# Performance work log

Measured on AMD Instinct MI355X. Metric: run time of the kernel, lower is better.

The kernel has to match this reference:

```python
import jax, jax.numpy as jnp
import numpy as np


def setup_inputs() -> dict:
    key = jax.random.key(0)
    k1, k2, k3, k4, k5 = jax.random.split(key, 5)
    N, M, K = 200000, 50, 4
    T = 1000.0
    ti = jnp.sort(jax.random.uniform(k1, (N,), dtype=jnp.float32) * T)
    mi = jax.random.randint(k2, (N,), 0, M, dtype=jnp.int64)
    mu_at_events = jax.random.uniform(k3, (N,), dtype=jnp.float32) * 0.5 + 0.05
    alpha = jax.random.uniform(k4, (K, M, M), dtype=jnp.float32) * 0.1
    gamma = jax.random.uniform(k5, (K,), dtype=jnp.float32) * 2.0 + 0.5
    return {"ti": ti, "mi": mi, "mu_at_events": mu_at_events, "alpha": alpha, "gamma": gamma}


def _hawkes_logsum(ti, mi, mu_at_events, alpha, gamma):
    # ti: [N] sorted event times; mi: [N] event types in [0, M)
    # alpha: [K, M, M]; gamma: [K]; mu_at_events: [N]
    N = ti.shape[0]
    M = alpha.shape[1]
    # inter-event gaps; dt[0] = 0 so the first event has zero excitation state
    dt = jnp.concatenate([jnp.zeros((1,), ti.dtype), ti[1:] - ti[:-1]])  # [N]
    a = jnp.exp(-gamma[None, :] * dt[:, None])  # [N, K] decay factors
    # one-hot of the PREVIOUS event's type (row 0 is all-zero, matching e_mi)
    prev_onehot = jnp.zeros((N, M), ti.dtype).at[jnp.arange(1, N), mi[:-1]].set(1.0)
    b = a[:, None, :] * prev_onehot[:, :, None]  # [N, M, K]

    # linear recurrence S_i = a_i * S_{i-1} + b_i via associative scan
    # combine((a1,b1),(a2,b2)) = (a1*a2, a2*b1 + b2)
    def combine(x, y):
        a1, b1 = x
        a2, b2 = y
        return (a1 * a2, a2[:, None, :] * b1 + b2)

    _, S = jax.lax.associative_scan(combine, (a, b))  # S: [N, M, K]
    # S[i, m, k] = sum_{j < i, m_j = m} exp(-gamma_k (t_i - t_j))
    alpha_at = alpha[:, mi, :]  # [K, N, M] rows of alpha for each event's type
    lam = mu_at_events + jnp.einsum('knm,nmk,k->n', alpha_at, S, gamma)  # [N]
    return jnp.sum(jnp.log(lam))


def reference(ti, mi, mu_at_events, alpha, gamma):
    return _hawkes_logsum(ti, mi, mu_at_events, alpha, gamma)
```

## Files before the change

### kernel.cpp

```cpp
#include <hip/hip_runtime.h>

#define CHUNK 256
#define MM 50
#define KK 4
#define STATE (MM*KK)
#define ASTRIDE 51
#define SUP 32
#define NSMAX 26
#define NSUB 8
#define SUBSZ 32
#define GMAX 1024

__device__ int      g_ticket;
__device__ unsigned g_flag[GMAX];
__device__ unsigned g_sflag[64];
__device__ float    g_chunkB[GMAX * STATE];
__device__ float    g_superB[64 * STATE];

__device__ __forceinline__ unsigned short f2bf(float x) {
  unsigned u = __float_as_uint(x);
  u += 0x7fffu + ((u >> 16) & 1u);
  return (unsigned short)(u >> 16);
}
__device__ __forceinline__ float bflo(unsigned u) { return __uint_as_float(u << 16); }
__device__ __forceinline__ float bfhi(unsigned u) { return __uint_as_float(u & 0xffff0000u); }

__device__ __forceinline__ void st_agent(float* p, float v) {
  __hip_atomic_store(p, v, __ATOMIC_RELAXED, __HIP_MEMORY_SCOPE_AGENT);
}
__device__ __forceinline__ float ld_agent(const float* p) {
  return __hip_atomic_load(p, __ATOMIC_RELAXED, __HIP_MEMORY_SCOPE_AGENT);
}

__global__ __launch_bounds__(512) void hawkes_fused(
    const float* __restrict__ ti, const int* __restrict__ mi,
    const float* __restrict__ mu, const float* __restrict__ alpha,
    const float* __restrict__ gamma, float* __restrict__ out, int N, int G) {
  int tid = threadIdx.x;
  __shared__ int vid_s;
  __shared__ uint2 P[MM * ASTRIDE];
  __shared__ __align__(16) float4 Fj[CHUNK];
  __shared__ int   cj[CHUNK];
  __shared__ __align__(16) float Q[NSUB][STATE];
  __shared__ float red8[8];
  __shared__ float teL[SUP];
  __shared__ float tlast[NSMAX];
  __shared__ float S_lds[STATE];
  __shared__ __align__(16) float R_lds[MM * 20];

  if (tid == 0) vid_s = atomicAdd(&g_ticket, 1);

  int g = blockIdx.x;
  int l = g * CHUNK;
  int r = min(N, l + CHUNK);
  int cnt = r - l;
  int sup = g / SUP;
  int g0 = sup * SUP;
  int e = tid >> 1;
  int h = tid & 1;

  float gk0 = gamma[0], gk1 = gamma[1], gk2 = gamma[2], gk3 = gamma[3];

  for (int i = tid; i < NSUB * STATE; i += 512) ((float*)Q)[i] = 0.f;

  if (tid < SUP) {
    int c = g0 + tid;
    if (c < G) teL[tid] = ti[min(N, (c + 1) * CHUNK) - 1];
  } else if (tid >= 64 && tid < 64 + NSMAX) {
    int s = tid - 64;
    if (s < sup) tlast[s] = ti[min(N, (s + 1) * SUP * CHUNK) - 1];
  }

  float t_ref = ti[(g == 0) ? 0 : (l - 1)];
  bool valid = false;
  int myc = 0;
  float4 myF = make_float4(0.f, 0.f, 0.f, 0.f);
  if (tid < CHUNK) {
    int j = l - 1 + tid;
    valid = (j >= 0) && (j <= r - 2);
    if (valid) {
      myc = mi[j];
      float tj = ti[j] - t_ref;
      myF = make_float4(__expf(gk0 * tj), __expf(gk1 * tj),
                        __expf(gk2 * tj), __expf(gk3 * tj));
    }
    cj[tid] = myc;
    Fj[tid] = myF;
  }
  __syncthreads();

  if (valid) {
    float* q = &Q[tid >> 5][myc * KK];
    atomicAdd(q + 0, myF.x); atomicAdd(q + 1, myF.y);
    atomicAdd(q + 2, myF.z); atomicAdd(q + 3, myF.w);
  }
  __syncthreads();

  float gk = (tid & 2) ? ((tid & 1) ? gk3 : gk2) : ((tid & 1) ? gk1 : gk0);
  float Bv = 0.f, t_end = 0.f;
  if (tid < STATE) {
    t_end = teL[g - g0];
    float tot = 0.f;
    #pragma unroll
    for (int q = 0; q < NSUB; ++q) tot += Q[q][tid];
    Bv = __expf(-gk * (t_end - t_ref)) * tot;
    st_agent(&g_chunkB[g * STATE + tid], Bv);
    float run = 0.f;
    #pragma unroll
    for (int q = 0; q < NSUB; ++q) {
      float tq = Q[q][tid];
      Q[q][tid] = run;
      run += tq;
    }
  }
  if (g == 0 && tid == 0) st_agent(out, 0.f);

  for (int idx = tid; idx < MM * MM; idx += 512) {
    int c = idx / MM, cp = idx - c * MM;
    float a0 = gk0 * alpha[idx];
    float a1 = gk1 * alpha[2500 + idx];
    float a2 = gk2 * alpha[5000 + idx];
    float a3 = gk3 * alpha[7500 + idx];
    P[c * ASTRIDE + cp] =
        make_uint2((unsigned)f2bf(a0) | ((unsigned)f2bf(a1) << 16),
                   (unsigned)f2bf(a2) | ((unsigned)f2bf(a3) << 16));
  }
  __syncthreads();
  unsigned DONE = (unsigned)(vid_s / G) + 1u;
  if (tid == 0) {
    asm volatile("s_waitcnt vmcnt(0)" ::: "memory");
    __hip_atomic_store(&g_flag[g], DONE, __ATOMIC_RELAXED, __HIP_MEMORY_SCOPE_AGENT);
  }

  int nloc = g - g0;
  bool closer = (nloc == SUP - 1) || (g == G - 1);
  float S = 0.f;

  if (closer) {
    if (tid < nloc) {
      while (__hip_atomic_load(&g_flag[g0 + tid], __ATOMIC_RELAXED,
                               __HIP_MEMORY_SCOPE_AGENT) != DONE)
        __builtin_amdgcn_s_sleep(2);
    }
    __syncthreads();
    if (tid < STATE) {
      #pragma unroll 8
      for (int u = 0; u < nloc; ++u)
        S += __expf(-gk * (t_ref - teL[u])) * ld_agent(&g_chunkB[(g0 + u) * STATE + tid]);
      st_agent(&g_superB[sup * STATE + tid], __expf(-gk * (t_end - t_ref)) * S + Bv);
    }
    __syncthreads();
    if (tid == 0) {
      asm volatile("s_waitcnt vmcnt(0)" ::: "memory");
      __hip_atomic_store(&g_sflag[sup], DONE, __ATOMIC_RELAXED, __HIP_MEMORY_SCOPE_AGENT);
    }
  }

  int c_n = (e < cnt) ? mi[l + e] : 0;
  int rowb = c_n * ASTRIDE;
  float tn = 0.f, mun = 0.f;
  if (h == 0 && e < cnt) { tn = ti[l + e] - t_ref; mun = mu[l + e]; }
  float4 acc = make_float4(0.f, 0.f, 0.f, 0.f);
  if (e < cnt) {
    const float4* wb = (const float4*)&Q[e >> 5][0];
    if (e >= SUBSZ) {
      int mlo = h * 25, mhi = mlo + 25;
      #pragma unroll 5
      for (int m = mlo; m < mhi; ++m) {
        uint2 p = P[rowb + m];
        float4 w = wb[m];
        acc.x += bflo(p.x) * w.x; acc.y += bfhi(p.x) * w.y;
        acc.z += bflo(p.y) * w.z; acc.w += bfhi(p.y) * w.w;
      }
    }
    #pragma unroll 4
    for (int s = (e & ~(SUBSZ - 1)) + h; s <= e; s += 2) {
      uint2 p = P[rowb + cj[s]];
      float4 f = Fj[s];
      acc.x += bflo(p.x) * f.x; acc.y += bfhi(p.x) * f.y;
      acc.z += bflo(p.y) * f.z; acc.w += bfhi(p.y) * f.w;
    }
  }
  acc.x += __shfl_xor(acc.x, 1, 64);
  acc.y += __shfl_xor(acc.y, 1, 64);
  acc.z += __shfl_xor(acc.z, 1, 64);
  acc.w += __shfl_xor(acc.w, 1, 64);

  if (!closer) {
    if (tid < nloc) {
      while (__hip_atomic_load(&g_flag[g0 + tid], __ATOMIC_RELAXED,
                               __HIP_MEMORY_SCOPE_AGENT) != DONE)
        __builtin_amdgcn_s_sleep(2);
    }
    __syncthreads();
    if (tid < STATE) {
      #pragma unroll 8
      for (int u = 0; u < nloc; ++u)
        S += __expf(-gk * (t_ref - teL[u])) * ld_agent(&g_chunkB[(g0 + u) * STATE + tid]);
    }
  }
  if (tid < sup) {
    while (__hip_atomic_load(&g_sflag[tid], __ATOMIC_RELAXED,
                             __HIP_MEMORY_SCOPE_AGENT) != DONE)
      __builtin_amdgcn_s_sleep(2);
  }
  __syncthreads();
  if (tid < STATE) {
    #pragma unroll 8
    for (int s = 0; s < sup; ++s)
      S += __expf(-gk * (t_ref - tlast[s])) * ld_agent(&g_superB[s * STATE + tid]);
    S_lds[tid] = S;
  }
  __syncthreads();

  if (tid < STATE) {
    int c = tid >> 2, k = tid & 3;
    float rv = 0.f;
    #pragma unroll 5
    for (int m = 0; m < MM; ++m) {
      uint2 p = P[c * ASTRIDE + m];
      unsigned w = (k & 2) ? p.y : p.x;
      float pv = (k & 1) ? bfhi(w) : bflo(w);
      rv += pv * S_lds[m * KK + k];
    }
    R_lds[c * 20 + k] = rv;
  }
  __syncthreads();

  float local = 0.f;
  if (h == 0 && e < cnt) {
    float4 rv = *(const float4*)&R_lds[c_n * 20];
    float lam = mun
              + __expf(-gk0 * tn) * (acc.x + rv.x)
              + __expf(-gk1 * tn) * (acc.y + rv.y)
              + __expf(-gk2 * tn) * (acc.z + rv.z)
              + __expf(-gk3 * tn) * (acc.w + rv.w);
    local = __logf(lam);
  }
  #pragma unroll
  for (int off = 32; off > 0; off >>= 1)
    local += __shfl_down(local, off, 64);
  if ((tid & 63) == 0) red8[tid >> 6] = local;
  __syncthreads();
  if (tid == 0) {
    float acc8 = 0.f;
    #pragma unroll
    for (int w = 0; w < 8; ++w) acc8 += red8[w];
    atomicAdd(out, acc8);
  }
}

extern "C" void kernel_launch(void* const* d_in, const int* in_sizes, int n_in,
                              void* d_out, int out_size, void* d_ws, size_t ws_size,
                              hipStream_t stream) {
  const float* ti    = (const float*)d_in[0];
  const int*   mi    = (const int*)d_in[1];
  const float* mu    = (const float*)d_in[2];
  const float* alpha = (const float*)d_in[3];
  const float* gamma = (const float*)d_in[4];
  float* out = (float*)d_out;
  int N = in_sizes[0];
  int G = (N + CHUNK - 1) / CHUNK;
  if (G > GMAX) return;

  hawkes_fused<<<G, 512, 0, stream>>>(ti, mi, mu, alpha, gamma, out, N, G);
}
```

Baseline: 94.00 us.

## Process two chunks per block with one thread per event

Each 512-thread block now handles two adjacent 256-event chunks, with one thread per event instead of two threads splitting each event's sum. The block count is halved. This shortens the cross-block flag chain, and the second chunk's carry-in state is derived locally from the first. The flag publish is also moved ahead of the alpha table build, so dependent blocks can start sooner. In exchange, each thread does twice the serial inner-loop work, which lengthens per-thread latency.

```diff
diff --git a/kernel.cpp b/kernel.cpp
--- a/kernel.cpp
+++ b/kernel.cpp
@@ -7,7 +7,6 @@
 #define ASTRIDE 51
 #define SUP 32
 #define NSMAX 26
-#define NSUB 8
 #define SUBSZ 32
 #define GMAX 1024
 
@@ -31,62 +30,71 @@
 __device__ __forceinline__ float ld_agent(const float* p) {
   return __hip_atomic_load(p, __ATOMIC_RELAXED, __HIP_MEMORY_SCOPE_AGENT);
 }
+__device__ __forceinline__ void spin_flag(unsigned* p, unsigned want) {
+  while (__hip_atomic_load(p, __ATOMIC_RELAXED, __HIP_MEMORY_SCOPE_AGENT) != want)
+    __builtin_amdgcn_s_sleep(2);
+}
 
 __global__ __launch_bounds__(512) void hawkes_fused(
     const float* __restrict__ ti, const int* __restrict__ mi,
     const float* __restrict__ mu, const float* __restrict__ alpha,
-    const float* __restrict__ gamma, float* __restrict__ out, int N, int G) {
+    const float* __restrict__ gamma, float* __restrict__ out,
+    int N, int G, int NB) {
   int tid = threadIdx.x;
   __shared__ int vid_s;
   __shared__ uint2 P[MM * ASTRIDE];
-  __shared__ __align__(16) float4 Fj[CHUNK];
-  __shared__ int   cj[CHUNK];
-  __shared__ __align__(16) float Q[NSUB][STATE];
+  __shared__ __align__(16) float4 Fj[2 * CHUNK];
+  __shared__ int   cj[2 * CHUNK];
+  __shared__ __align__(16) float Q[16][STATE];
   __shared__ float red8[8];
   __shared__ float teL[SUP];
   __shared__ float tlast[NSMAX];
-  __shared__ float S_lds[STATE];
-  __shared__ __align__(16) float R_lds[MM * 20];
+  __shared__ float SldsA[STATE];
+  __shared__ float SldsB[STATE];
+  __shared__ __align__(16) float RA[MM * 20];
+  __shared__ __align__(16) float RB[MM * 20];
 
   if (tid == 0) vid_s = atomicAdd(&g_ticket, 1);
 
-  int g = blockIdx.x;
-  int l = g * CHUNK;
-  int r = min(N, l + CHUNK);
-  int cnt = r - l;
-  int sup = g / SUP;
-  int g0 = sup * SUP;
-  int e = tid >> 1;
-  int h = tid & 1;
+  int b = blockIdx.x;
+  int gA = 2 * b, gB = gA + 1;
+  bool hasB = (gB < G);
+  int lA = gA * CHUNK;
+  int sup = gA / SUP;
+  int g0c = sup * SUP;
+  int half = tid >> 8;
+  int cidx = tid & 255;
 
   float gk0 = gamma[0], gk1 = gamma[1], gk2 = gamma[2], gk3 = gamma[3];
-
-  for (int i = tid; i < NSUB * STATE; i += 512) ((float*)Q)[i] = 0.f;
+  float gkc = (tid & 2) ? ((tid & 1) ? gk3 : gk2) : ((tid & 1) ? gk1 : gk0);
+
+  for (int i = tid; i < 16 * STATE; i += 512) ((float*)Q)[i] = 0.f;
 
   if (tid < SUP) {
-    int c = g0 + tid;
+    int c = g0c + tid;
     if (c < G) teL[tid] = ti[min(N, (c + 1) * CHUNK) - 1];
   } else if (tid >= 64 && tid < 64 + NSMAX) {
     int s = tid - 64;
     if (s < sup) tlast[s] = ti[min(N, (s + 1) * SUP * CHUNK) - 1];
   }
 
-  float t_ref = ti[(g == 0) ? 0 : (l - 1)];
-  bool valid = false;
+  float t_refA = ti[(gA == 0) ? 0 : (lA - 1)];
+  float t_refB = ti[min(N, lA + CHUNK) - 1];
+  float t_ref = half ? t_refB : t_refA;
+
+  int j = lA - 1 + tid;
+  int rX = min(N, lA + (half + 1) * CHUNK);
+  bool valid = (j >= 0) && (j <= rX - 2);
   int myc = 0;
   float4 myF = make_float4(0.f, 0.f, 0.f, 0.f);
-  if (tid < CHUNK) {
-    int j = l - 1 + tid;
-    valid = (j >= 0) && (j <= r - 2);
-    if (valid) {
-      myc = mi[j];
-      float tj = ti[j] - t_ref;
-      myF = make_float4(__expf(gk0 * tj), __expf(gk1 * tj),
-                        __expf(gk2 * tj), __expf(gk3 * tj));
-    }
-    cj[tid] = myc;
-    Fj[tid] = myF;
-  }
+  if (valid) {
+    myc = mi[j];
+    float tj = ti[j] - t_ref;
+    myF = make_float4(__expf(gk0 * tj), __expf(gk1 * tj),
+                      __expf(gk2 * tj), __expf(gk3 * tj));
+  }
+  cj[tid] = myc;
+  Fj[tid] = myF;
   __syncthreads();
 
   if (valid) {
@@ -96,24 +104,33 @@
   }
   __syncthreads();
 
-  float gk = (tid & 2) ? ((tid & 1) ? gk3 : gk2) : ((tid & 1) ? gk1 : gk0);
-  float Bv = 0.f, t_end = 0.f;
-  if (tid < STATE) {
-    t_end = teL[g - g0];
+  bool sumr = (cidx < STATE) && (half == 0 || hasB);
+  int gX = half ? gB : gA;
+  float Bv = 0.f, dX = 0.f;
+  if (sumr) {
     float tot = 0.f;
     #pragma unroll
-    for (int q = 0; q < NSUB; ++q) tot += Q[q][tid];
-    Bv = __expf(-gk * (t_end - t_ref)) * tot;
-    st_agent(&g_chunkB[g * STATE + tid], Bv);
+    for (int q = 0; q < 8; ++q) tot += Q[half * 8 + q][cidx];
+    dX = __expf(-gkc * (teL[gX - g0c] - t_ref));
+    Bv = dX * tot;
+    st_agent(&g_chunkB[(size_t)gX * STATE + cidx], Bv);
     float run = 0.f;
     #pragma unroll
-    for (int q = 0; q < NSUB; ++q) {
-      float tq = Q[q][tid];
-      Q[q][tid] = run;
+    for (int q = 0; q < 8; ++q) {
+      float tq = Q[half * 8 + q][cidx];
+      Q[half * 8 + q][cidx] = run;
       run += tq;
     }
   }
-  if (g == 0 && tid == 0) st_agent(out, 0.f);
+  if (b == 0 && tid == 0) st_agent(out, 0.f);
+  __syncthreads();
+  unsigned DONE = (unsigned)(vid_s / NB) + 1u;
+  if (tid == 0) {
+    asm volatile("s_waitcnt vmcnt(0)" ::: "memory");
+    __hip_atomic_store(&g_flag[gA], DONE, __ATOMIC_RELAXED, __HIP_MEMORY_SCOPE_AGENT);
+    if (hasB)
+      __hip_atomic_store(&g_flag[gB], DONE, __ATOMIC_RELAXED, __HIP_MEMORY_SCOPE_AGENT);
+  }
 
   for (int idx = tid; idx < MM * MM; idx += 512) {
     int c = idx / MM, cp = idx - c * MM;
@@ -125,29 +142,29 @@
         make_uint2((unsigned)f2bf(a0) | ((unsigned)f2bf(a1) << 16),
                    (unsigned)f2bf(a2) | ((unsigned)f2bf(a3) << 16));
   }
-  __syncthreads();
-  unsigned DONE = (unsigned)(vid_s / G) + 1u;
-  if (tid == 0) {
-    asm volatile("s_waitcnt vmcnt(0)" ::: "memory");
-    __hip_atomic_store(&g_flag[g], DONE, __ATOMIC_RELAXED, __HIP_MEMORY_SCOPE_AGENT);
-  }
-
-  int nloc = g - g0;
-  bool closer = (nloc == SUP - 1) || (g == G - 1);
+
+  int n = lA + tid;
+  bool en = (n < N);
+  int c_n = en ? mi[n] : 0;
+  float tn = 0.f, mun = 0.f;
+  if (en) { tn = ti[n] - t_ref; mun = mu[n]; }
+
+  int nlocA = gA - g0c;
+  bool closer = (hasB && (gB - g0c == SUP - 1)) || (b == NB - 1);
   float S = 0.f;
 
   if (closer) {
-    if (tid < nloc) {
-      while (__hip_atomic_load(&g_flag[g0 + tid], __ATOMIC_RELAXED,
-                               __HIP_MEMORY_SCOPE_AGENT) != DONE)
-        __builtin_amdgcn_s_sleep(2);
-    }
+    if (tid < nlocA) spin_flag(&g_flag[g0c + tid], DONE);
     __syncthreads();
     if (tid < STATE) {
-      #pragma unroll 8
-      for (int u = 0; u < nloc; ++u)
-        S += __expf(-gk * (t_ref - teL[u])) * ld_agent(&g_chunkB[(g0 + u) * STATE + tid]);
-      st_agent(&g_superB[sup * STATE + tid], __expf(-gk * (t_end - t_ref)) * S + Bv);
+      #pragma unroll 16
+      for (int u = 0; u < nlocA; ++u)
+        S += __expf(-gkc * (t_refA - teL[u])) * ld_agent(&g_chunkB[(size_t)(g0c + u) * STATE + tid]);
+      SldsB[tid] = dX * S + Bv;
+    }
+    __syncthreads();
+    if (sumr && half) {
+      st_agent(&g_superB[(size_t)sup * STATE + cidx], dX * SldsB[cidx] + Bv);
     }
     __syncthreads();
     if (tid == 0) {
@@ -155,81 +172,70 @@
       __hip_atomic_store(&g_sflag[sup], DONE, __ATOMIC_RELAXED, __HIP_MEMORY_SCOPE_AGENT);
     }
   }
-
-  int c_n = (e < cnt) ? mi[l + e] : 0;
-  int rowb = c_n * ASTRIDE;
-  float tn = 0.f, mun = 0.f;
-  if (h == 0 && e < cnt) { tn = ti[l + e] - t_ref; mun = mu[l + e]; }
+  __syncthreads();
+
   float4 acc = make_float4(0.f, 0.f, 0.f, 0.f);
-  if (e < cnt) {
-    const float4* wb = (const float4*)&Q[e >> 5][0];
-    if (e >= SUBSZ) {
-      int mlo = h * 25, mhi = mlo + 25;
-      #pragma unroll 5
-      for (int m = mlo; m < mhi; ++m) {
+  if (en) {
+    int rowb = c_n * ASTRIDE;
+    const float4* wb = (const float4*)&Q[tid >> 5][0];
+    if (cidx >= SUBSZ) {
+      #pragma unroll 10
+      for (int m = 0; m < MM; ++m) {
         uint2 p = P[rowb + m];
         float4 w = wb[m];
         acc.x += bflo(p.x) * w.x; acc.y += bfhi(p.x) * w.y;
         acc.z += bflo(p.y) * w.z; acc.w += bfhi(p.y) * w.w;
       }
     }
+    int base = tid & ~(SUBSZ - 1);
     #pragma unroll 4
-    for (int s = (e & ~(SUBSZ - 1)) + h; s <= e; s += 2) {
+    for (int s = base; s <= tid; ++s) {
       uint2 p = P[rowb + cj[s]];
       float4 f = Fj[s];
       acc.x += bflo(p.x) * f.x; acc.y += bfhi(p.x) * f.y;
       acc.z += bflo(p.y) * f.z; acc.w += bfhi(p.y) * f.w;
     }
   }
-  acc.x += __shfl_xor(acc.x, 1, 64);
-  acc.y += __shfl_xor(acc.y, 1, 64);
-  acc.z += __shfl_xor(acc.z, 1, 64);
-  acc.w += __shfl_xor(acc.w, 1, 64);
 
   if (!closer) {
-    if (tid < nloc) {
-      while (__hip_atomic_load(&g_flag[g0 + tid], __ATOMIC_RELAXED,
-                               __HIP_MEMORY_SCOPE_AGENT) != DONE)
-        __builtin_amdgcn_s_sleep(2);
-    }
+    if (tid < nlocA) spin_flag(&g_flag[g0c + tid], DONE);
     __syncthreads();
     if (tid < STATE) {
-      #pragma unroll 8
-      for (int u = 0; u < nloc; ++u)
-        S += __expf(-gk * (t_ref - teL[u])) * ld_agent(&g_chunkB[(g0 + u) * STATE + tid]);
-    }
-  }
-  if (tid < sup) {
-    while (__hip_atomic_load(&g_sflag[tid], __ATOMIC_RELAXED,
-                             __HIP_MEMORY_SCOPE_AGENT) != DONE)
-      __builtin_amdgcn_s_sleep(2);
-  }
+      #pragma unroll 16
+      for (int u = 0; u < nlocA; ++u)
+        S += __expf(-gkc * (t_refA - teL[u])) * ld_agent(&g_chunkB[(size_t)(g0c + u) * STATE + tid]);
+    }
+  }
+  if (tid < sup) spin_flag(&g_sflag[tid], DONE);
   __syncthreads();
   if (tid < STATE) {
-    #pragma unroll 8
+    #pragma unroll 16
     for (int s = 0; s < sup; ++s)
-      S += __expf(-gk * (t_ref - tlast[s])) * ld_agent(&g_superB[s * STATE + tid]);
-    S_lds[tid] = S;
-  }
-  __syncthreads();
-
-  if (tid < STATE) {
-    int c = tid >> 2, k = tid & 3;
+      S += __expf(-gkc * (t_refA - tlast[s])) * ld_agent(&g_superB[(size_t)s * STATE + tid]);
+    SldsA[tid] = S;
+    SldsB[tid] = dX * S + Bv;
+  }
+  __syncthreads();
+
+  if (sumr) {
+    int c = cidx >> 2, k = cidx & 3;
+    const float* Sx = half ? SldsB : SldsA;
     float rv = 0.f;
-    #pragma unroll 5
+    #pragma unroll 10
     for (int m = 0; m < MM; ++m) {
       uint2 p = P[c * ASTRIDE + m];
       unsigned w = (k & 2) ? p.y : p.x;
       float pv = (k & 1) ? bfhi(w) : bflo(w);
-      rv += pv * S_lds[m * KK + k];
-    }
-    R_lds[c * 20 + k] = rv;
+      rv += pv * Sx[m * KK + k];
+    }
+    (half ? RB : RA)[c * 20 + k] = rv;
   }
   __syncthreads();
 
   float local = 0.f;
-  if (h == 0 && e < cnt) {
-    float4 rv = *(const float4*)&R_lds[c_n * 20];
+  if (en) {
+    const float* Rx = half ? RB : RA;
+    float4 rv = *(const float4*)&Rx[c_n * 20];
     float lam = mun
               + __expf(-gk0 * tn) * (acc.x + rv.x)
               + __expf(-gk1 * tn) * (acc.y + rv.y)
@@ -262,6 +268,7 @@
   int N = in_sizes[0];
   int G = (N + CHUNK - 1) / CHUNK;
   if (G > GMAX) return;
-
-  hawkes_fused<<<G, 512, 0, stream>>>(ti, mi, mu, alpha, gamma, out, N, G);
-}
+  int NB = (G + 1) / 2;
+
+  hawkes_fused<<<NB, 512, 0, stream>>>(ti, mi, mu, alpha, gamma, out, N, G, NB);
+}
```

Measured after the change: 88.70 us. -5.6%, faster.
